# Kernel optimization log

Measured on AMD Instinct MI355X. Metric: run time of the kernel, lower is better.

## Reference

```python
import jax, jax.numpy as jnp
import numpy as np

HEADS = 16
HEAD_DIM = 64
EMB = HEADS * HEAD_DIM
MAX_REL = 512
B, L = 4, 1024


def _rel_indices(length_q, length_k):
    # Shaw-style clipped relative distance indices into the embeddings table
    dist = jnp.arange(length_k)[None, :] - jnp.arange(length_q)[:, None]
    return jnp.clip(dist, -MAX_REL, MAX_REL) + MAX_REL  # [Lq, Lk] in [0, 2*MAX_REL]


def setup_inputs() -> dict:
    key = jax.random.key(0)
    ks = jax.random.split(key, 16)
    d = {
        "query": jax.random.normal(ks[0], (B, L, EMB), jnp.float32),
        "key": jax.random.normal(ks[1], (B, L, EMB), jnp.float32),
        "value": jax.random.normal(ks[2], (B, L, EMB), jnp.float32),
        "mask": jnp.ones((B, 1, L, L), jnp.int32),
        # per-head Linear(head_dims, head_dims) weights stored torch-style [out, in]
        "Wq": jax.random.normal(ks[3], (HEAD_DIM, HEAD_DIM), jnp.float32) / np.sqrt(HEAD_DIM),
        "bq": jax.random.normal(ks[4], (HEAD_DIM,), jnp.float32) * 0.02,
        "Wk": jax.random.normal(ks[5], (HEAD_DIM, HEAD_DIM), jnp.float32) / np.sqrt(HEAD_DIM),
        "bk": jax.random.normal(ks[6], (HEAD_DIM,), jnp.float32) * 0.02,
        "Wv": jax.random.normal(ks[7], (HEAD_DIM, HEAD_DIM), jnp.float32) / np.sqrt(HEAD_DIM),
        "bv": jax.random.normal(ks[8], (HEAD_DIM,), jnp.float32) * 0.02,
        "Wfc": jax.random.normal(ks[9], (EMB, EMB), jnp.float32) / np.sqrt(EMB),
        "bfc": jax.random.normal(ks[10], (EMB,), jnp.float32) * 0.02,
        "rel_k_table": jax.random.normal(ks[11], (2 * MAX_REL + 1, HEAD_DIM), jnp.float32) * 0.02,
        "rel_v_table": jax.random.normal(ks[12], (2 * MAX_REL + 1, HEAD_DIM), jnp.float32) * 0.02,
    }
    return d


def reference(query, key, value, mask, Wq, bq, Wk, bk, Wv, bv, Wfc, bfc, rel_k_table, rel_v_table):
    b, lq, _ = query.shape
    lk = key.shape[1]
    # split heads then per-head linear projections (torch Linear: x @ W.T + b)
    q = query.reshape(b, lq, HEADS, HEAD_DIM) @ Wq.T + bq
    k = key.reshape(b, lk, HEADS, HEAD_DIM) @ Wk.T + bk
    v = value.reshape(b, lk, HEADS, HEAD_DIM) @ Wv.T + bv

    score = jnp.einsum('bqhd,bkhd->bhqk', q, k)  # [B,H,Lq,Lk]
    score = jnp.where(mask == 0, jnp.float32(-1e20), score)

    idx = _rel_indices(lq, lk)
    a_key = rel_k_table[idx]    # [Lq, Lk, D]
    a_val = rel_v_table[idx]    # [Lq, Lk, D]
    score = score + jnp.einsum('blhd,lrd->bhlr', q, a_key)

    attn = jax.nn.softmax(score / np.sqrt(HEAD_DIM), axis=-1)

    out = jnp.einsum('bhqv,bvhd->bqhd', attn, v)
    # original: einsum('brhl,hld->bhrd', attn[b,h,q,k], a_val[q,k,d]) -> [b,q,h,d]
    out = out + jnp.einsum('bhql,qld->bqhd', attn, a_val)
    out = out.reshape(b, lq, EMB)
    return out @ Wfc.T + bfc
```

## Files before the change

### kernel.cpp

```cpp
#include <hip/hip_runtime.h>
#include <hip/hip_bf16.h>

#define SEQ 1024
#define HEADS 16
#define HDIM 64
#define EMB 1024
#define TQ 16
#define PBS 1032
#define RELK_ROWS 1040
#define RELV_STRIDE 1032

typedef __bf16 bf16x8 __attribute__((ext_vector_type(8)));
typedef unsigned short u16x8 __attribute__((ext_vector_type(8)));
typedef float floatx4 __attribute__((ext_vector_type(4)));

static __device__ __forceinline__ unsigned short f2bu(float f) {
    unsigned u = __builtin_bit_cast(unsigned, f);
    u = (u + 0x7fffu + ((u >> 16) & 1u)) >> 16;
    return (unsigned short)u;
}
static __device__ __forceinline__ float b2f(unsigned short u) {
    unsigned v = ((unsigned)u) << 16;
    return __builtin_bit_cast(float, v);
}

__global__ __launch_bounds__(256) void sa_proj_kernel(
    const float* __restrict__ qin, const float* __restrict__ kin,
    const float* __restrict__ vin,
    const unsigned short* __restrict__ wqb, const unsigned short* __restrict__ wkb,
    const unsigned short* __restrict__ wvb,
    const float* __restrict__ bq, const float* __restrict__ bk,
    const float* __restrict__ bv_,
    unsigned short* __restrict__ qb, unsigned short* __restrict__ kb,
    unsigned short* __restrict__ vtb) {
    const int t = threadIdx.x;
    const int w = t >> 6, lane = t & 63;
    const int quad = lane >> 4, l16 = lane & 15;
    const int which = blockIdx.y;
    const int r0 = blockIdx.x * 16;
    const int bidx = r0 >> 10;
    const int l0 = r0 & 1023;
    const float* x = (which == 0) ? qin : (which == 1) ? kin : vin;
    const unsigned short* Wb = (which == 0) ? wqb : (which == 1) ? wkb : wvb;
    const float* bias = (which == 0) ? bq : (which == 1) ? bk : bv_;

    bf16x8 wf[4][2];
#pragma unroll
    for (int dt = 0; dt < 4; ++dt)
#pragma unroll
        for (int ks = 0; ks < 2; ++ks)
            wf[dt][ks] = *(const bf16x8*)(Wb + (size_t)(dt * 16 + l16) * 64 + ks * 32 + quad * 8);

    if (which < 2) {
        float biasd[4];
#pragma unroll
        for (int dt = 0; dt < 4; ++dt) biasd[dt] = bias[dt * 16 + l16];
        const float sc = (which == 0) ? 0.125f : 1.0f;
        unsigned short* dst = (which == 0) ? qb : kb;
        for (int hh = 0; hh < 4; ++hh) {
            const int h = w * 4 + hh;
            bf16x8 xf[2];
#pragma unroll
            for (int ks = 0; ks < 2; ++ks) {
                const float* xp = x + (size_t)(r0 + l16) * EMB + h * 64 + ks * 32 + quad * 8;
                float4 lo = *(const float4*)xp;
                float4 hi = *(const float4*)(xp + 4);
                u16x8 px;
                px[0] = f2bu(lo.x); px[1] = f2bu(lo.y); px[2] = f2bu(lo.z); px[3] = f2bu(lo.w);
                px[4] = f2bu(hi.x); px[5] = f2bu(hi.y); px[6] = f2bu(hi.z); px[7] = f2bu(hi.w);
                xf[ks] = __builtin_bit_cast(bf16x8, px);
            }
            floatx4 acc[4];
#pragma unroll
            for (int dt = 0; dt < 4; ++dt) acc[dt] = floatx4{0.f, 0.f, 0.f, 0.f};
#pragma unroll
            for (int dt = 0; dt < 4; ++dt)
#pragma unroll
                for (int ks = 0; ks < 2; ++ks)
                    acc[dt] = __builtin_amdgcn_mfma_f32_16x16x32_bf16(xf[ks], wf[dt][ks], acc[dt], 0, 0, 0);
            const int bh = bidx * HEADS + h;
#pragma unroll
            for (int dt = 0; dt < 4; ++dt)
#pragma unroll
                for (int i = 0; i < 4; ++i) {
                    const int lr = l0 + quad * 4 + i;
                    float val = (acc[dt][i] + biasd[dt]) * sc;
                    dst[((size_t)bh * SEQ + lr) * 64 + dt * 16 + l16] = f2bu(val);
                }
        }
    } else {
        float biasv[4][4];
#pragma unroll
        for (int dt = 0; dt < 4; ++dt)
#pragma unroll
            for (int i = 0; i < 4; ++i) biasv[dt][i] = bias[dt * 16 + quad * 4 + i];
        for (int hh = 0; hh < 4; ++hh) {
            const int h = w * 4 + hh;
            bf16x8 xf[2];
#pragma unroll
            for (int ks = 0; ks < 2; ++ks) {
                const float* xp = x + (size_t)(r0 + l16) * EMB + h * 64 + ks * 32 + quad * 8;
                float4 lo = *(const float4*)xp;
                float4 hi = *(const float4*)(xp + 4);
                u16x8 px;
                px[0] = f2bu(lo.x); px[1] = f2bu(lo.y); px[2] = f2bu(lo.z); px[3] = f2bu(lo.w);
                px[4] = f2bu(hi.x); px[5] = f2bu(hi.y); px[6] = f2bu(hi.z); px[7] = f2bu(hi.w);
                xf[ks] = __builtin_bit_cast(bf16x8, px);
            }
            floatx4 acc[4];
#pragma unroll
            for (int dt = 0; dt < 4; ++dt) acc[dt] = floatx4{0.f, 0.f, 0.f, 0.f};
#pragma unroll
            for (int dt = 0; dt < 4; ++dt)
#pragma unroll
                for (int ks = 0; ks < 2; ++ks)
                    acc[dt] = __builtin_amdgcn_mfma_f32_16x16x32_bf16(wf[dt][ks], xf[ks], acc[dt], 0, 0, 0);
            const int bh = bidx * HEADS + h;
#pragma unroll
            for (int dt = 0; dt < 4; ++dt)
#pragma unroll
                for (int i = 0; i < 4; ++i) {
                    const int d = dt * 16 + quad * 4 + i;
                    float val = acc[dt][i] + biasv[dt][i];
                    vtb[((size_t)bh * 64 + d) * SEQ + l0 + l16] = f2bu(val);
                }
        }
    }
}

#define NW (1024 * 1024)
#define NRK (RELK_ROWS * 64)
#define NRV (64 * RELV_STRIDE)
#define NWP (3 * 4096)
__global__ __launch_bounds__(256) void sa_prep_kernel(
    const float* __restrict__ Wfc, const float* __restrict__ relk,
    const float* __restrict__ relv,
    const float* __restrict__ Wq, const float* __restrict__ Wk,
    const float* __restrict__ Wv,
    unsigned short* __restrict__ wfcb, unsigned short* __restrict__ relkb,
    unsigned short* __restrict__ relvtb,
    unsigned short* __restrict__ wqb, unsigned short* __restrict__ wkb,
    unsigned short* __restrict__ wvb) {
    int i = blockIdx.x * 256 + threadIdx.x;
    if (i < NW) {
        wfcb[i] = f2bu(Wfc[i]);
    } else if (i < NW + NRK) {
        int j = i - NW;
        int r = j >> 6, d = j & 63;
        relkb[j] = (r <= 1024) ? f2bu(relk[r * 64 + d]) : 0;
    } else if (i < NW + NRK + NRV) {
        int j = i - NW - NRK;
        int d = j / RELV_STRIDE, c = j - d * RELV_STRIDE;
        relvtb[j] = (c <= 1024) ? f2bu(relv[c * 64 + d]) : 0;
    } else if (i < NW + NRK + NRV + NWP) {
        int j = i - NW - NRK - NRV;
        int which = j >> 12, e = j & 4095;
        const float* src = (which == 0) ? Wq : (which == 1) ? Wk : Wv;
        unsigned short* dst = (which == 0) ? wqb : (which == 1) ? wkb : wvb;
        dst[e] = f2bu(src[e]);
    }
}

__global__ __launch_bounds__(256) void sa_maskred1(const int* __restrict__ mask,
                                                   unsigned* __restrict__ part) {
    const int b = blockIdx.y, chunk = blockIdx.x;
    const int4* p = (const int4*)(mask + (size_t)b * (SEQ * SEQ) + chunk * 16384);
    int ok = 1;
    const int t = threadIdx.x;
#pragma unroll
    for (int i = 0; i < 16; ++i) {
        int4 v = p[t + i * 256];
        ok &= (v.x != 0 && v.y != 0 && v.z != 0 && v.w != 0) ? 1 : 0;
    }
    unsigned long long bal = __ballot(ok);
    __shared__ unsigned wok[4];
    if ((t & 63) == 0) wok[t >> 6] = (bal == ~0ull) ? 1u : 0u;
    __syncthreads();
    if (t == 0)
        part[b * 64 + chunk] = (wok[0] & wok[1] & wok[2] & wok[3]) ? 0xFFFFFFFFu : 0u;
}
__global__ void sa_maskred2(const unsigned* __restrict__ part, unsigned* __restrict__ flags) {
    int t = threadIdx.x;
    if (t < 4) {
        unsigned f = 0xFFFFFFFFu;
        for (int i = 0; i < 64; ++i) f &= part[t * 64 + i];
        flags[t] = f;
    }
}

__global__ __launch_bounds__(512, 4) void sa_attn_kernel(
    const unsigned short* __restrict__ qb, const unsigned short* __restrict__ kb,
    const unsigned short* __restrict__ vtb, const int* __restrict__ mask,
    const unsigned short* __restrict__ relkb, const unsigned short* __restrict__ relvtb,
    const unsigned* __restrict__ flags, unsigned short* __restrict__ aob) {
    __shared__ unsigned short PbA[TQ * PBS];
    __shared__ unsigned short PbB[TQ * PBS];
    __shared__ float Ored[TQ * 64];
    __shared__ float wred[4][128];
    __shared__ float invS[TQ], lowS[TQ], highS[TQ];

    const int tid = threadIdx.x;
    const int w = tid >> 6, lane = tid & 63;
    const int quad = lane >> 4, l16 = lane & 15;
    const int bid = blockIdx.x;
    const int bh = bid >> 6;
    const int q0 = (bid & 63) * TQ;
    const int b = bh >> 4, h = bh & 15;
    const bool mfull = (flags[b] == 0xFFFFFFFFu);

    bf16x8 aq[2];
    {
        const unsigned short* qrow = qb + ((size_t)bh * SEQ + q0 + l16) * 64;
        aq[0] = *(const bf16x8*)(qrow + quad * 8);
        aq[1] = *(const bf16x8*)(qrow + 32 + quad * 8);
    }

    unsigned short* RS = PbB;
    for (int rt = w; rt < 65; rt += 8) {
        floatx4 racc = {0.f, 0.f, 0.f, 0.f};
#pragma unroll
        for (int ks = 0; ks < 2; ++ks) {
            bf16x8 bf = *(const bf16x8*)(relkb + (size_t)(rt * 16 + l16) * 64 + ks * 32 + quad * 8);
            racc = __builtin_amdgcn_mfma_f32_16x16x32_bf16(aq[ks], bf, racc, 0, 0, 0);
        }
        const int rcol = rt * 16 + l16;
        if (rcol <= 1024) {
#pragma unroll
            for (int i = 0; i < 4; ++i)
                RS[(quad * 4 + i) * PBS + rcol] = f2bu(racc[i]);
        }
    }
    __syncthreads();

    const int kbase = w * 128;
    floatx4 acc[8];
#pragma unroll
    for (int tt = 0; tt < 8; ++tt) acc[tt] = floatx4{0.f, 0.f, 0.f, 0.f};
#pragma unroll
    for (int tt = 0; tt < 8; ++tt) {
#pragma unroll
        for (int ks = 0; ks < 2; ++ks) {
            bf16x8 bf = *(const bf16x8*)(
                kb + ((size_t)bh * SEQ + kbase + tt * 16 + l16) * 64 + ks * 32 + quad * 8);
            acc[tt] = __builtin_amdgcn_mfma_f32_16x16x32_bf16(aq[ks], bf, acc[tt], 0, 0, 0);
        }
    }
    float rmax[4] = {-3.0e38f, -3.0e38f, -3.0e38f, -3.0e38f};
    if (mfull) {
#pragma unroll
        for (int tt = 0; tt < 8; ++tt) {
            const int k = kbase + tt * 16 + l16;
#pragma unroll
            for (int i = 0; i < 4; ++i) {
                const int row = quad * 4 + i;
                const int q = q0 + row;
                int r = min(512, max(-512, k - q)) + 512;
                float s = acc[tt][i] + b2f(RS[row * PBS + r]);
                acc[tt][i] = s;
                rmax[i] = fmaxf(rmax[i], s);
            }
        }
    } else {
#pragma unroll
        for (int tt = 0; tt < 8; ++tt) {
            const int k = kbase + tt * 16 + l16;
#pragma unroll
            for (int i = 0; i < 4; ++i) {
                const int row = quad * 4 + i;
                const int q = q0 + row;
                int r = min(512, max(-512, k - q)) + 512;
                float s = acc[tt][i] + b2f(RS[row * PBS + r]);
                int m = mask[(size_t)b * (SEQ * SEQ) + (size_t)q * SEQ + k];
                s = (m == 0) ? -1e20f : s;
                acc[tt][i] = s;
                rmax[i] = fmaxf(rmax[i], s);
            }
        }
    }
#pragma unroll
    for (int i = 0; i < 4; ++i) {
#pragma unroll
        for (int o = 1; o < 16; o <<= 1) rmax[i] = fmaxf(rmax[i], __shfl_xor(rmax[i], o));
    }
    if (l16 == 0) {
#pragma unroll
        for (int i = 0; i < 4; ++i) wred[0][(quad * 4 + i) * 8 + w] = rmax[i];
    }
    __syncthreads();

    for (int g = tid; g < TQ * 129; g += 512) {
        int row = g / 129, s2 = g - row * 129;
        *(uint4*)&PbB[row * PBS + s2 * 8] = make_uint4(0u, 0u, 0u, 0u);
    }
    float mx[4];
#pragma unroll
    for (int i = 0; i < 4; ++i) {
        const int row = quad * 4 + i;
        float4 a = *(float4*)&wred[0][row * 8];
        float4 c = *(float4*)&wred[0][row * 8 + 4];
        mx[i] = fmaxf(fmaxf(fmaxf(a.x, a.y), fmaxf(a.z, a.w)),
                      fmaxf(fmaxf(c.x, c.y), fmaxf(c.z, c.w)));
    }
    __syncthreads();

    float ssum[4] = {0.f, 0.f, 0.f, 0.f};
    float slow[4] = {0.f, 0.f, 0.f, 0.f};
    float shigh[4] = {0.f, 0.f, 0.f, 0.f};
#pragma unroll
    for (int tt = 0; tt < 8; ++tt) {
        const int k = kbase + tt * 16 + l16;
#pragma unroll
        for (int i = 0; i < 4; ++i) {
            const int row = quad * 4 + i;
            const int q = q0 + row;
            float p = __expf(acc[tt][i] - mx[i]);
            ssum[i] += p;
            const int dist = k - q;
            slow[i] += (dist <= -512) ? p : 0.f;
            shigh[i] += (dist >= 512) ? p : 0.f;
            unsigned short pv = f2bu(p);
            PbA[row * PBS + k] = pv;
            const int c = dist + 512;
            if ((unsigned)(c - 1) < 1023u) PbB[row * PBS + c] = pv;
        }
    }
#pragma unroll
    for (int i = 0; i < 4; ++i) {
#pragma unroll
        for (int o = 1; o < 16; o <<= 1) {
            ssum[i] += __shfl_xor(ssum[i], o);
            slow[i] += __shfl_xor(slow[i], o);
            shigh[i] += __shfl_xor(shigh[i], o);
        }
    }
    if (l16 == 0) {
#pragma unroll
        for (int i = 0; i < 4; ++i) {
            const int row = quad * 4 + i;
            wred[1][row * 8 + w] = ssum[i];
            wred[2][row * 8 + w] = slow[i];
            wred[3][row * 8 + w] = shigh[i];
        }
    }
    __syncthreads();
    if (tid < TQ) {
        float s = 0.f, lo = 0.f, hi = 0.f;
#pragma unroll
        for (int j = 0; j < 8; ++j) {
            s += wred[1][tid * 8 + j];
            lo += wred[2][tid * 8 + j];
            hi += wred[3][tid * 8 + j];
        }
        invS[tid] = 1.f / s;
        lowS[tid] = lo;
        highS[tid] = hi;
    }
    __syncthreads();

    const int d0 = (w & 3) * 16;
    const int khalf = w >> 2;
    floatx4 accA = {0.f, 0.f, 0.f, 0.f};
    floatx4 accB = {0.f, 0.f, 0.f, 0.f};
    const unsigned short* vbase = vtb + ((size_t)bh * 64 + d0 + l16) * SEQ;
    const unsigned short* rbase = relvtb + (size_t)(d0 + l16) * RELV_STRIDE;
    for (int ks = khalf * 16; ks < khalf * 16 + 16; ++ks) {
        const int co = ks * 32 + quad * 8;
        bf16x8 ap = *(const bf16x8*)&PbA[l16 * PBS + co];
        bf16x8 bv = *(const bf16x8*)(vbase + co);
        accA = __builtin_amdgcn_mfma_f32_16x16x32_bf16(ap, bv, accA, 0, 0, 0);
        bf16x8 ar = *(const bf16x8*)&PbB[l16 * PBS + co];
        bf16x8 br = *(const bf16x8*)(rbase + co);
        accB = __builtin_amdgcn_mfma_f32_16x16x32_bf16(ar, br, accB, 0, 0, 0);
    }
    if (w >= 4) {
#pragma unroll
        for (int i = 0; i < 4; ++i)
            Ored[(quad * 4 + i) * 64 + d0 + l16] = accA[i] + accB[i];
    }
    __syncthreads();
    if (w < 4) {
        const float rv0 = b2f(rbase[0]);
        const float rv1 = b2f(rbase[1024]);
#pragma unroll
        for (int i = 0; i < 4; ++i) {
            const int row = quad * 4 + i;
            float val = accA[i] + accB[i] + Ored[row * 64 + d0 + l16] +
                        lowS[row] * rv0 + highS[row] * rv1;
            val *= invS[row];
            aob[((size_t)(b * SEQ + q0 + row)) * EMB + h * 64 + d0 + l16] = f2bu(val);
        }
    }
}

__global__ __launch_bounds__(256, 2) void sa_fc_kernel(
    const unsigned short* __restrict__ A, const unsigned short* __restrict__ W,
    const float* __restrict__ bias, float* __restrict__ out) {
    const int t = threadIdx.x;
    const int w = t >> 6, lane = t & 63;
    const int quad = lane >> 4, l16 = lane & 15;
    const int mw = blockIdx.x * 64 + (w & 1) * 32;
    const int nw = blockIdx.y * 256 + (w >> 1) * 128;

    floatx4 acc[2][8];
#pragma unroll
    for (int mt = 0; mt < 2; ++mt)
#pragma unroll
        for (int j = 0; j < 8; ++j) acc[mt][j] = floatx4{0.f, 0.f, 0.f, 0.f};
    float bj[8];
#pragma unroll
    for (int j = 0; j < 8; ++j) bj[j] = bias[nw + j * 16 + l16];

    for (int ks = 0; ks < 32; ++ks) {
        const int co = ks * 32 + quad * 8;
        bf16x8 af0 = *(const bf16x8*)(A + (size_t)(mw + l16) * EMB + co);
        bf16x8 af1 = *(const bf16x8*)(A + (size_t)(mw + 16 + l16) * EMB + co);
#pragma unroll
        for (int j = 0; j < 8; ++j) {
            bf16x8 bf = *(const bf16x8*)(W + (size_t)(nw + j * 16 + l16) * EMB + co);
            acc[0][j] = __builtin_amdgcn_mfma_f32_16x16x32_bf16(af0, bf, acc[0][j], 0, 0, 0);
            acc[1][j] = __builtin_amdgcn_mfma_f32_16x16x32_bf16(af1, bf, acc[1][j], 0, 0, 0);
        }
    }
#pragma unroll
    for (int mt = 0; mt < 2; ++mt)
#pragma unroll
        for (int j = 0; j < 8; ++j) {
            const int col = nw + j * 16 + l16;
#pragma unroll
            for (int i = 0; i < 4; ++i) {
                const size_t row = mw + mt * 16 + quad * 4 + i;
                out[row * EMB + col] = acc[mt][j][i] + bj[j];
            }
        }
}

extern "C" void kernel_launch(void* const* d_in, const int* in_sizes, int n_in,
                              void* d_out, int out_size, void* d_ws, size_t ws_size,
                              hipStream_t stream) {
    const float* query = (const float*)d_in[0];
    const float* key = (const float*)d_in[1];
    const float* value = (const float*)d_in[2];
    const int* mask = (const int*)d_in[3];
    const float* Wq = (const float*)d_in[4];
    const float* bq = (const float*)d_in[5];
    const float* Wk = (const float*)d_in[6];
    const float* bk = (const float*)d_in[7];
    const float* Wv = (const float*)d_in[8];
    const float* bv = (const float*)d_in[9];
    const float* Wfc = (const float*)d_in[10];
    const float* bfc = (const float*)d_in[11];
    const float* relk = (const float*)d_in[12];
    const float* relv = (const float*)d_in[13];
    float* out = (float*)d_out;

    char* base = (char*)d_ws;
    const size_t MB = (size_t)1 << 20;
    unsigned short* qb = (unsigned short*)(base + 0 * MB);
    unsigned short* kb = (unsigned short*)(base + 8 * MB);
    unsigned short* vtb = (unsigned short*)(base + 16 * MB);
    unsigned short* aob = (unsigned short*)(base + 24 * MB);
    unsigned short* wfcb = (unsigned short*)(base + 32 * MB);
    unsigned short* relkb = (unsigned short*)(base + 34 * MB);
    unsigned short* relvtb = (unsigned short*)(base + 34 * MB + 135168);
    unsigned short* wqb = (unsigned short*)(base + 34 * MB + 270336);
    unsigned short* wkb = (unsigned short*)(base + 34 * MB + 278528);
    unsigned short* wvb = (unsigned short*)(base + 34 * MB + 286720);
    unsigned* flags = (unsigned*)(base + 34 * MB + 294912);
    unsigned* part = (unsigned*)(base + 34 * MB + 295936);

    sa_prep_kernel<<<(NW + NRK + NRV + NWP + 255) / 256, 256, 0, stream>>>(
        Wfc, relk, relv, Wq, Wk, Wv, wfcb, relkb, relvtb, wqb, wkb, wvb);
    sa_proj_kernel<<<dim3(256, 3), 256, 0, stream>>>(
        query, key, value, wqb, wkb, wvb, bq, bk, bv, qb, kb, vtb);
    sa_maskred1<<<dim3(64, 4), 256, 0, stream>>>(mask, part);
    sa_maskred2<<<1, 64, 0, stream>>>(part, flags);
    sa_attn_kernel<<<64 * 64, 512, 0, stream>>>(
        qb, kb, vtb, mask, relkb, relvtb, flags, aob);
    sa_fc_kernel<<<dim3(64, 4), 256, 0, stream>>>(aob, wfcb, bfc, out);
}
```

Baseline: 422.2 us.

## Split attention over key halves with flash-style combine and windowed relative tiles

The attention kernel now splits each query tile's keys into two halves, so it launches twice as many blocks, each half the size. Each block writes partial outputs in fp16 along with its row max and sum, and a new combine kernel merges the halves. The relative-key score and relative-value MFMA loops are restricted to the window of clipped distances that a key half can reach, which cuts redundant work and LDS. The mask reduction is folded into the prep kernel to save a launch, and bf16 conversion now uses the native cast. The trade-offs are an extra kernel, a partial-output round trip through global memory, and fp16 precision for the partials.

```diff
diff --git a/kernel.cpp b/kernel.cpp
--- a/kernel.cpp
+++ b/kernel.cpp
@@ -1,23 +1,24 @@
 #include <hip/hip_runtime.h>
 #include <hip/hip_bf16.h>
+#include <hip/hip_fp16.h>
 
 #define SEQ 1024
 #define HEADS 16
 #define HDIM 64
 #define EMB 1024
 #define TQ 16
-#define PBS 1032
+#define KH 512
+#define PBA_S 520
+#define PBB_S 552
 #define RELK_ROWS 1040
-#define RELV_STRIDE 1032
+#define RELV_S 1064
 
 typedef __bf16 bf16x8 __attribute__((ext_vector_type(8)));
-typedef unsigned short u16x8 __attribute__((ext_vector_type(8)));
 typedef float floatx4 __attribute__((ext_vector_type(4)));
 
 static __device__ __forceinline__ unsigned short f2bu(float f) {
-    unsigned u = __builtin_bit_cast(unsigned, f);
-    u = (u + 0x7fffu + ((u >> 16) & 1u)) >> 16;
-    return (unsigned short)u;
+    __bf16 h = (__bf16)f;
+    return __builtin_bit_cast(unsigned short, h);
 }
 static __device__ __forceinline__ float b2f(unsigned short u) {
     unsigned v = ((unsigned)u) << 16;
@@ -65,10 +66,10 @@
                 const float* xp = x + (size_t)(r0 + l16) * EMB + h * 64 + ks * 32 + quad * 8;
                 float4 lo = *(const float4*)xp;
                 float4 hi = *(const float4*)(xp + 4);
-                u16x8 px;
+                unsigned short px[8];
                 px[0] = f2bu(lo.x); px[1] = f2bu(lo.y); px[2] = f2bu(lo.z); px[3] = f2bu(lo.w);
                 px[4] = f2bu(hi.x); px[5] = f2bu(hi.y); px[6] = f2bu(hi.z); px[7] = f2bu(hi.w);
-                xf[ks] = __builtin_bit_cast(bf16x8, px);
+                xf[ks] = *(bf16x8*)px;
             }
             floatx4 acc[4];
 #pragma unroll
@@ -102,10 +103,10 @@
                 const float* xp = x + (size_t)(r0 + l16) * EMB + h * 64 + ks * 32 + quad * 8;
                 float4 lo = *(const float4*)xp;
                 float4 hi = *(const float4*)(xp + 4);
-                u16x8 px;
+                unsigned short px[8];
                 px[0] = f2bu(lo.x); px[1] = f2bu(lo.y); px[2] = f2bu(lo.z); px[3] = f2bu(lo.w);
                 px[4] = f2bu(hi.x); px[5] = f2bu(hi.y); px[6] = f2bu(hi.z); px[7] = f2bu(hi.w);
-                xf[ks] = __builtin_bit_cast(bf16x8, px);
+                xf[ks] = *(bf16x8*)px;
             }
             floatx4 acc[4];
 #pragma unroll
@@ -130,55 +131,58 @@
 
 #define NW (1024 * 1024)
 #define NRK (RELK_ROWS * 64)
-#define NRV (64 * RELV_STRIDE)
+#define NRV (64 * RELV_S)
 #define NWP (3 * 4096)
+#define CONV_BLOCKS ((NW + NRK + NRV + NWP) / 256)
 __global__ __launch_bounds__(256) void sa_prep_kernel(
     const float* __restrict__ Wfc, const float* __restrict__ relk,
     const float* __restrict__ relv,
     const float* __restrict__ Wq, const float* __restrict__ Wk,
-    const float* __restrict__ Wv,
+    const float* __restrict__ Wv, const int* __restrict__ mask,
     unsigned short* __restrict__ wfcb, unsigned short* __restrict__ relkb,
     unsigned short* __restrict__ relvtb,
     unsigned short* __restrict__ wqb, unsigned short* __restrict__ wkb,
-    unsigned short* __restrict__ wvb) {
-    int i = blockIdx.x * 256 + threadIdx.x;
-    if (i < NW) {
-        wfcb[i] = f2bu(Wfc[i]);
-    } else if (i < NW + NRK) {
-        int j = i - NW;
-        int r = j >> 6, d = j & 63;
-        relkb[j] = (r <= 1024) ? f2bu(relk[r * 64 + d]) : 0;
-    } else if (i < NW + NRK + NRV) {
-        int j = i - NW - NRK;
-        int d = j / RELV_STRIDE, c = j - d * RELV_STRIDE;
-        relvtb[j] = (c <= 1024) ? f2bu(relv[c * 64 + d]) : 0;
-    } else if (i < NW + NRK + NRV + NWP) {
-        int j = i - NW - NRK - NRV;
-        int which = j >> 12, e = j & 4095;
-        const float* src = (which == 0) ? Wq : (which == 1) ? Wk : Wv;
-        unsigned short* dst = (which == 0) ? wqb : (which == 1) ? wkb : wvb;
-        dst[e] = f2bu(src[e]);
-    }
-}
-
-__global__ __launch_bounds__(256) void sa_maskred1(const int* __restrict__ mask,
-                                                   unsigned* __restrict__ part) {
-    const int b = blockIdx.y, chunk = blockIdx.x;
-    const int4* p = (const int4*)(mask + (size_t)b * (SEQ * SEQ) + chunk * 16384);
-    int ok = 1;
+    unsigned short* __restrict__ wvb, unsigned* __restrict__ part) {
+    const int bx = blockIdx.x;
     const int t = threadIdx.x;
-#pragma unroll
-    for (int i = 0; i < 16; ++i) {
-        int4 v = p[t + i * 256];
-        ok &= (v.x != 0 && v.y != 0 && v.z != 0 && v.w != 0) ? 1 : 0;
-    }
-    unsigned long long bal = __ballot(ok);
-    __shared__ unsigned wok[4];
-    if ((t & 63) == 0) wok[t >> 6] = (bal == ~0ull) ? 1u : 0u;
-    __syncthreads();
-    if (t == 0)
-        part[b * 64 + chunk] = (wok[0] & wok[1] & wok[2] & wok[3]) ? 0xFFFFFFFFu : 0u;
-}
+    if (bx < CONV_BLOCKS) {
+        int i = bx * 256 + t;
+        if (i < NW) {
+            wfcb[i] = f2bu(Wfc[i]);
+        } else if (i < NW + NRK) {
+            int j = i - NW;
+            int r = j >> 6, d = j & 63;
+            relkb[j] = (r <= 1024) ? f2bu(relk[r * 64 + d]) : 0;
+        } else if (i < NW + NRK + NRV) {
+            int j = i - NW - NRK;
+            int d = j / RELV_S, c = j - d * RELV_S;
+            relvtb[j] = (c <= 1024) ? f2bu(relv[c * 64 + d]) : 0;
+        } else {
+            int j = i - NW - NRK - NRV;
+            int which = j >> 12, e = j & 4095;
+            const float* src = (which == 0) ? Wq : (which == 1) ? Wk : Wv;
+            unsigned short* dst = (which == 0) ? wqb : (which == 1) ? wkb : wvb;
+            dst[e] = f2bu(src[e]);
+        }
+    } else {
+        const int mb = bx - CONV_BLOCKS;
+        const int b = mb >> 6, chunk = mb & 63;
+        const int4* p = (const int4*)(mask + (size_t)b * (SEQ * SEQ) + chunk * 16384);
+        int ok = 1;
+#pragma unroll
+        for (int i = 0; i < 16; ++i) {
+            int4 v = p[t + i * 256];
+            ok &= (v.x != 0 && v.y != 0 && v.z != 0 && v.w != 0) ? 1 : 0;
+        }
+        unsigned long long bal = __ballot(ok);
+        __shared__ unsigned wok[4];
+        if ((t & 63) == 0) wok[t >> 6] = (bal == ~0ull) ? 1u : 0u;
+        __syncthreads();
+        if (t == 0)
+            part[b * 64 + chunk] = (wok[0] & wok[1] & wok[2] & wok[3]) ? 0xFFFFFFFFu : 0u;
+    }
+}
+
 __global__ void sa_maskred2(const unsigned* __restrict__ part, unsigned* __restrict__ flags) {
     int t = threadIdx.x;
     if (t < 4) {
@@ -188,25 +192,34 @@
     }
 }
 
-__global__ __launch_bounds__(512, 4) void sa_attn_kernel(
+__global__ __launch_bounds__(512, 8) void sa_attn_kernel(
     const unsigned short* __restrict__ qb, const unsigned short* __restrict__ kb,
     const unsigned short* __restrict__ vtb, const int* __restrict__ mask,
     const unsigned short* __restrict__ relkb, const unsigned short* __restrict__ relvtb,
-    const unsigned* __restrict__ flags, unsigned short* __restrict__ aob) {
-    __shared__ unsigned short PbA[TQ * PBS];
-    __shared__ unsigned short PbB[TQ * PBS];
+    const unsigned* __restrict__ flags, __half* __restrict__ Opart,
+    float2* __restrict__ ms) {
+    __shared__ __align__(16) unsigned short PbA[TQ * PBA_S];
+    __shared__ __align__(16) unsigned short PbB[TQ * PBB_S];
     __shared__ float Ored[TQ * 64];
     __shared__ float wred[4][128];
-    __shared__ float invS[TQ], lowS[TQ], highS[TQ];
+    __shared__ float lowS[TQ], highS[TQ];
 
     const int tid = threadIdx.x;
     const int w = tid >> 6, lane = tid & 63;
     const int quad = lane >> 4, l16 = lane & 15;
     const int bid = blockIdx.x;
-    const int bh = bid >> 6;
-    const int q0 = (bid & 63) * TQ;
-    const int b = bh >> 4, h = bh & 15;
+    const int hf = bid & 1;
+    const int qt = (bid >> 1) & 63;
+    const int bh = bid >> 7;
+    const int q0 = qt * TQ;
+    const int k0 = hf * KH;
+    const int b = bh >> 4;
     const bool mfull = (flags[b] == 0xFFFFFFFFu);
+
+    const int cmin = min(512, max(-512, k0 - (q0 + 15))) + 512;
+    const int cmax = min(512, max(-512, k0 + 511 - q0)) + 512;
+    const int rsb = cmin & ~15;
+    const int cb0 = cmin & ~7;
 
     bf16x8 aq[2];
     {
@@ -215,29 +228,31 @@
         aq[1] = *(const bf16x8*)(qrow + 32 + quad * 8);
     }
 
-    unsigned short* RS = PbB;
-    for (int rt = w; rt < 65; rt += 8) {
-        floatx4 racc = {0.f, 0.f, 0.f, 0.f};
-#pragma unroll
-        for (int ks = 0; ks < 2; ++ks) {
-            bf16x8 bf = *(const bf16x8*)(relkb + (size_t)(rt * 16 + l16) * 64 + ks * 32 + quad * 8);
-            racc = __builtin_amdgcn_mfma_f32_16x16x32_bf16(aq[ks], bf, racc, 0, 0, 0);
-        }
-        const int rcol = rt * 16 + l16;
-        if (rcol <= 1024) {
-#pragma unroll
-            for (int i = 0; i < 4; ++i)
-                RS[(quad * 4 + i) * PBS + rcol] = f2bu(racc[i]);
+    {
+        const int rt_lo = cmin >> 4, rt_hi = cmax >> 4;
+        for (int rt = rt_lo + w; rt <= rt_hi; rt += 8) {
+            floatx4 racc = {0.f, 0.f, 0.f, 0.f};
+#pragma unroll
+            for (int ks = 0; ks < 2; ++ks) {
+                bf16x8 bf = *(const bf16x8*)(relkb + (size_t)(rt * 16 + l16) * 64 + ks * 32 + quad * 8);
+                racc = __builtin_amdgcn_mfma_f32_16x16x32_bf16(aq[ks], bf, racc, 0, 0, 0);
+            }
+            const int rcol = rt * 16 + l16;
+            if (rcol <= cmax) {
+#pragma unroll
+                for (int i = 0; i < 4; ++i)
+                    PbB[(quad * 4 + i) * PBB_S + (rcol - rsb)] = f2bu(racc[i]);
+            }
         }
     }
     __syncthreads();
 
-    const int kbase = w * 128;
-    floatx4 acc[8];
-#pragma unroll
-    for (int tt = 0; tt < 8; ++tt) acc[tt] = floatx4{0.f, 0.f, 0.f, 0.f};
-#pragma unroll
-    for (int tt = 0; tt < 8; ++tt) {
+    const int kbase = k0 + w * 64;
+    floatx4 acc[4];
+#pragma unroll
+    for (int tt = 0; tt < 4; ++tt) acc[tt] = floatx4{0.f, 0.f, 0.f, 0.f};
+#pragma unroll
+    for (int tt = 0; tt < 4; ++tt) {
 #pragma unroll
         for (int ks = 0; ks < 2; ++ks) {
             bf16x8 bf = *(const bf16x8*)(
@@ -248,28 +263,28 @@
     float rmax[4] = {-3.0e38f, -3.0e38f, -3.0e38f, -3.0e38f};
     if (mfull) {
 #pragma unroll
-        for (int tt = 0; tt < 8; ++tt) {
+        for (int tt = 0; tt < 4; ++tt) {
             const int k = kbase + tt * 16 + l16;
 #pragma unroll
             for (int i = 0; i < 4; ++i) {
                 const int row = quad * 4 + i;
                 const int q = q0 + row;
                 int r = min(512, max(-512, k - q)) + 512;
-                float s = acc[tt][i] + b2f(RS[row * PBS + r]);
+                float s = acc[tt][i] + b2f(PbB[row * PBB_S + (r - rsb)]);
                 acc[tt][i] = s;
                 rmax[i] = fmaxf(rmax[i], s);
             }
         }
     } else {
 #pragma unroll
-        for (int tt = 0; tt < 8; ++tt) {
+        for (int tt = 0; tt < 4; ++tt) {
             const int k = kbase + tt * 16 + l16;
 #pragma unroll
             for (int i = 0; i < 4; ++i) {
                 const int row = quad * 4 + i;
                 const int q = q0 + row;
                 int r = min(512, max(-512, k - q)) + 512;
-                float s = acc[tt][i] + b2f(RS[row * PBS + r]);
+                float s = acc[tt][i] + b2f(PbB[row * PBB_S + (r - rsb)]);
                 int m = mask[(size_t)b * (SEQ * SEQ) + (size_t)q * SEQ + k];
                 s = (m == 0) ? -1e20f : s;
                 acc[tt][i] = s;
@@ -288,9 +303,9 @@
     }
     __syncthreads();
 
-    for (int g = tid; g < TQ * 129; g += 512) {
-        int row = g / 129, s2 = g - row * 129;
-        *(uint4*)&PbB[row * PBS + s2 * 8] = make_uint4(0u, 0u, 0u, 0u);
+    for (int g = tid; g < TQ * (PBB_S / 8); g += 512) {
+        int row = g / (PBB_S / 8), j = g - row * (PBB_S / 8);
+        *(uint4*)&PbB[row * PBB_S + j * 8] = make_uint4(0u, 0u, 0u, 0u);
     }
     float mx[4];
 #pragma unroll
@@ -307,7 +322,7 @@
     float slow[4] = {0.f, 0.f, 0.f, 0.f};
     float shigh[4] = {0.f, 0.f, 0.f, 0.f};
 #pragma unroll
-    for (int tt = 0; tt < 8; ++tt) {
+    for (int tt = 0; tt < 4; ++tt) {
         const int k = kbase + tt * 16 + l16;
 #pragma unroll
         for (int i = 0; i < 4; ++i) {
@@ -319,9 +334,9 @@
             slow[i] += (dist <= -512) ? p : 0.f;
             shigh[i] += (dist >= 512) ? p : 0.f;
             unsigned short pv = f2bu(p);
-            PbA[row * PBS + k] = pv;
+            PbA[row * PBA_S + (k - k0)] = pv;
             const int c = dist + 512;
-            if ((unsigned)(c - 1) < 1023u) PbB[row * PBS + c] = pv;
+            if ((unsigned)(c - 1) < 1023u) PbB[row * PBB_S + (c - cb0)] = pv;
         }
     }
 #pragma unroll
@@ -344,32 +359,39 @@
     }
     __syncthreads();
     if (tid < TQ) {
+        float m = wred[0][tid * 8];
         float s = 0.f, lo = 0.f, hi = 0.f;
 #pragma unroll
         for (int j = 0; j < 8; ++j) {
+            m = fmaxf(m, wred[0][tid * 8 + j]);
             s += wred[1][tid * 8 + j];
             lo += wred[2][tid * 8 + j];
             hi += wred[3][tid * 8 + j];
         }
-        invS[tid] = 1.f / s;
         lowS[tid] = lo;
         highS[tid] = hi;
+        const int R = bh * SEQ + q0 + tid;
+        ms[(size_t)R * 2 + hf] = make_float2(m, s);
     }
     __syncthreads();
 
     const int d0 = (w & 3) * 16;
-    const int khalf = w >> 2;
+    const int kg = w >> 2;
     floatx4 accA = {0.f, 0.f, 0.f, 0.f};
     floatx4 accB = {0.f, 0.f, 0.f, 0.f};
-    const unsigned short* vbase = vtb + ((size_t)bh * 64 + d0 + l16) * SEQ;
-    const unsigned short* rbase = relvtb + (size_t)(d0 + l16) * RELV_STRIDE;
-    for (int ks = khalf * 16; ks < khalf * 16 + 16; ++ks) {
+    const unsigned short* vbase = vtb + ((size_t)bh * 64 + d0 + l16) * SEQ + k0;
+    const unsigned short* rbase = relvtb + (size_t)(d0 + l16) * RELV_S;
+    for (int ks = kg; ks < 16; ks += 2) {
         const int co = ks * 32 + quad * 8;
-        bf16x8 ap = *(const bf16x8*)&PbA[l16 * PBS + co];
+        bf16x8 ap = *(const bf16x8*)&PbA[l16 * PBA_S + co];
         bf16x8 bv = *(const bf16x8*)(vbase + co);
         accA = __builtin_amdgcn_mfma_f32_16x16x32_bf16(ap, bv, accA, 0, 0, 0);
-        bf16x8 ar = *(const bf16x8*)&PbB[l16 * PBS + co];
-        bf16x8 br = *(const bf16x8*)(rbase + co);
+    }
+    const int nksB = ((cmax - cb0) >> 5) + 1;
+    for (int ks = kg; ks < nksB; ks += 2) {
+        const int co = ks * 32 + quad * 8;
+        bf16x8 ar = *(const bf16x8*)&PbB[l16 * PBB_S + co];
+        bf16x8 br = *(const bf16x8*)(rbase + cb0 + co);
         accB = __builtin_amdgcn_mfma_f32_16x16x32_bf16(ar, br, accB, 0, 0, 0);
     }
     if (w >= 4) {
@@ -384,12 +406,30 @@
 #pragma unroll
         for (int i = 0; i < 4; ++i) {
             const int row = quad * 4 + i;
+            const int R = bh * SEQ + q0 + row;
             float val = accA[i] + accB[i] + Ored[row * 64 + d0 + l16] +
                         lowS[row] * rv0 + highS[row] * rv1;
-            val *= invS[row];
-            aob[((size_t)(b * SEQ + q0 + row)) * EMB + h * 64 + d0 + l16] = f2bu(val);
-        }
-    }
+            Opart[((size_t)R * 2 + hf) * 64 + d0 + l16] = __float2half(val);
+        }
+    }
+}
+
+__global__ __launch_bounds__(256) void sa_combine_kernel(
+    const __half* __restrict__ Opart, const float2* __restrict__ ms,
+    unsigned short* __restrict__ aob) {
+    const int tid = threadIdx.x;
+    const int R = blockIdx.x * 4 + (tid >> 6);
+    const int d = tid & 63;
+    float2 s0 = ms[(size_t)R * 2 + 0];
+    float2 s1 = ms[(size_t)R * 2 + 1];
+    float m = fmaxf(s0.x, s1.x);
+    float a0 = __expf(s0.x - m), a1 = __expf(s1.x - m);
+    float inv = 1.f / (s0.y * a0 + s1.y * a1);
+    float O0 = __half2float(Opart[((size_t)R * 2 + 0) * 64 + d]);
+    float O1 = __half2float(Opart[((size_t)R * 2 + 1) * 64 + d]);
+    float val = (O0 * a0 + O1 * a1) * inv;
+    const int bh = R >> 10, q = R & 1023, b = bh >> 4, h = bh & 15;
+    aob[((size_t)b * SEQ + q) * EMB + h * 64 + d] = f2bu(val);
 }
 
 __global__ __launch_bounds__(256, 2) void sa_fc_kernel(
@@ -461,20 +501,22 @@
     unsigned short* aob = (unsigned short*)(base + 24 * MB);
     unsigned short* wfcb = (unsigned short*)(base + 32 * MB);
     unsigned short* relkb = (unsigned short*)(base + 34 * MB);
-    unsigned short* relvtb = (unsigned short*)(base + 34 * MB + 135168);
-    unsigned short* wqb = (unsigned short*)(base + 34 * MB + 270336);
-    unsigned short* wkb = (unsigned short*)(base + 34 * MB + 278528);
-    unsigned short* wvb = (unsigned short*)(base + 34 * MB + 286720);
-    unsigned* flags = (unsigned*)(base + 34 * MB + 294912);
-    unsigned* part = (unsigned*)(base + 34 * MB + 295936);
-
-    sa_prep_kernel<<<(NW + NRK + NRV + NWP + 255) / 256, 256, 0, stream>>>(
-        Wfc, relk, relv, Wq, Wk, Wv, wfcb, relkb, relvtb, wqb, wkb, wvb);
+    unsigned short* relvtb = (unsigned short*)(base + 34 * MB + 262144);
+    unsigned short* wqb = (unsigned short*)(base + 34 * MB + 524288);
+    unsigned short* wkb = (unsigned short*)(base + 34 * MB + 532480);
+    unsigned short* wvb = (unsigned short*)(base + 34 * MB + 540672);
+    unsigned* flags = (unsigned*)(base + 34 * MB + 548864);
+    unsigned* part = (unsigned*)(base + 34 * MB + 552960);
+    float2* ms = (float2*)(base + 35 * MB);
+    __half* Opart = (__half*)(base + 36 * MB);
+
+    sa_prep_kernel<<<CONV_BLOCKS + 256, 256, 0, stream>>>(
+        Wfc, relk, relv, Wq, Wk, Wv, mask, wfcb, relkb, relvtb, wqb, wkb, wvb, part);
     sa_proj_kernel<<<dim3(256, 3), 256, 0, stream>>>(
         query, key, value, wqb, wkb, wvb, bq, bk, bv, qb, kb, vtb);
-    sa_maskred1<<<dim3(64, 4), 256, 0, stream>>>(mask, part);
     sa_maskred2<<<1, 64, 0, stream>>>(part, flags);
-    sa_attn_kernel<<<64 * 64, 512, 0, stream>>>(
-        qb, kb, vtb, mask, relkb, relvtb, flags, aob);
+    sa_attn_kernel<<<64 * 64 * 2, 512, 0, stream>>>(
+        qb, kb, vtb, mask, relkb, relvtb, flags, Opart, ms);
+    sa_combine_kernel<<<(4 * HEADS * SEQ) / 4, 256, 0, stream>>>(Opart, ms, aob);
     sa_fc_kernel<<<dim3(64, 4), 256, 0, stream>>>(aob, wfcb, bfc, out);
 }
```

Result: faster. 412.0 us (-2.4%).
